# Kernel optimization log

Hardware: AMD Instinct MI355X
Metric: run time of the kernel (lower is better)

The kernel has to match this reference:

```python
import jax, jax.numpy as jnp
import numpy as np

N_BITS = 14
L = 1 << N_BITS
B, C_IN, C_OUT = 32, 32, 64

def _neigh_idx():
    # (L, n_bits): index j flipped at bit b -> j ^ (1<<b)
    s = jnp.arange(L)
    return jnp.stack([s ^ (1 << b) for b in range(N_BITS)], axis=1)

def setup_inputs() -> dict:
    key = jax.random.key(0)
    k1, k2, k3, k4 = jax.random.split(key, 4)
    x = jax.random.normal(k1, (B, C_IN, L), dtype=jnp.float32)
    w_self = jnp.ones((), dtype=jnp.float32)
    w_bits = jax.random.normal(k2, (N_BITS,), dtype=jnp.float32) * 0.1
    # Conv1d(kernel_size=1) weight squeezed to (C_out, C_in)
    mix_w = jax.random.normal(k3, (C_OUT, C_IN), dtype=jnp.float32) * (1.0 / np.sqrt(C_IN))
    mix_b = jax.random.normal(k4, (C_OUT,), dtype=jnp.float32) * 0.01
    return {"x": x, "w_self": w_self, "w_bits": w_bits, "mix_w": mix_w, "mix_b": mix_b}

def reference(x, w_self, w_bits, mix_w, mix_b):
    n_bits = w_bits.shape[0]
    idx = _neigh_idx()                          # (L, n_bits), int32
    xn = x[:, :, idx]                           # (B, C, L, n_bits) XOR-neighbor gather
    neigh_sum = jnp.einsum('bclk,k->bcl', xn, w_bits)
    y = w_self * x + neigh_sum
    y = y / (1.0 + n_bits)                      # agg == 'mean'
    # 1x1 conv mix: (B,C,L) x (C_out,C_in) -> (B,C_out,L)
    return jnp.einsum('bcl,oc->bol', y, mix_w) + mix_b[None, :, None]
```

## Files before the change

### kernel.cpp

```cpp
#include <hip/hip_runtime.h>

#define TILE  256
#define CIN   32
#define COUT  64
#define LSIZE 16384
#define NBITS 14

typedef float f32x4   __attribute__((ext_vector_type(4)));
typedef float vfloat4 __attribute__((ext_vector_type(4)));

__global__ __launch_bounds__(256, 4)
void hamming_fused(const float* __restrict__ x,
                   const float* __restrict__ w_self,
                   const float* __restrict__ w_bits,
                   const float* __restrict__ mix_w,
                   const float* __restrict__ mix_b,
                   float* __restrict__ out)
{
    __shared__ float xs[CIN][TILE];
    __shared__ float mws[CIN][COUT];

    const int tid  = threadIdx.x;
    const int lane = tid & 63;
    const int wv   = tid >> 6;

    const int d    = blockIdx.x;
    const int xcd  = d & 7;
    const int j    = d >> 3;
    const int b    = xcd * 4 + (j >> 6);
    const int tile = j & 63;
    const int base = tile * TILE;
    const float* xb = x + (size_t)b * CIN * LSIZE;

    #pragma unroll
    for (int i = 0; i < (CIN * COUT) / 256; ++i) {
        int g = tid + i * 256;
        int o = g >> 5, c = g & 31;
        mws[c][o] = mix_w[g];
    }

    #pragma unroll
    for (int i = 0; i < 8; ++i) {
        const int r = wv + i * 4;
        const float* src = xb + (size_t)r * LSIZE + base + lane * 4;
        __builtin_amdgcn_global_load_lds(
            (const __attribute__((address_space(1))) void*)src,
            (__attribute__((address_space(3))) void*)&xs[r][lane * 4],
            16, 0, 0);
    }

    const float ws = w_self[0];
    float wb[NBITS];
    #pragma unroll
    for (int k = 0; k < NBITS; ++k) wb[k] = w_bits[k];

    __syncthreads();

    const int c0   = wv * 8;
    const int colb = lane * 4;

    f32x4 yv[8];
    #pragma unroll
    for (int cc = 0; cc < 8; cc += 2) {
        f32x4 pf[2][6];
        #pragma unroll
        for (int u = 0; u < 2; ++u) {
            const float* xr = xb + (size_t)(c0 + cc + u) * LSIZE;
            #pragma unroll
            for (int kk = 0; kk < 6; ++kk)
                pf[u][kk] = *(const f32x4*)(xr + ((base ^ (TILE << kk)) + colb));
        }
        #pragma unroll
        for (int u = 0; u < 2; ++u) {
            const int c = c0 + cc + u;
            const f32x4 s = *(const f32x4*)&xs[c][colb];
            f32x4 a = s * ws;
            a.x += wb[0] * s.y; a.y += wb[0] * s.x; a.z += wb[0] * s.w; a.w += wb[0] * s.z;
            a.x += wb[1] * s.z; a.y += wb[1] * s.w; a.z += wb[1] * s.x; a.w += wb[1] * s.y;
            #pragma unroll
            for (int k = 2; k < 8; ++k) {
                const f32x4 t = *(const f32x4*)&xs[c][colb ^ (1 << k)];
                a += wb[k] * t;
            }
            #pragma unroll
            for (int kk = 0; kk < 6; ++kk)
                a += wb[8 + kk] * pf[u][kk];
            yv[cc + u] = a * (1.0f / 15.0f);
        }
    }
    __syncthreads();

    #pragma unroll
    for (int cc = 0; cc < 8; ++cc)
        *(f32x4*)&xs[c0 + cc][colb] = yv[cc];
    __syncthreads();

    const int tx  = tid & 63;
    const int ty  = tid >> 6;
    const int cb2 = tx << 2;
    const int o0  = ty * 16;

    float4 acc[16];
    #pragma unroll
    for (int jj = 0; jj < 16; ++jj) {
        float bias = mix_b[o0 + jj];
        acc[jj] = make_float4(bias, bias, bias, bias);
    }

    #pragma unroll 4
    for (int c = 0; c < CIN; ++c) {
        float4 yc = *(float4*)&xs[c][cb2];
        #pragma unroll
        for (int j4 = 0; j4 < 4; ++j4) {
            float4 m = *(float4*)&mws[c][o0 + j4 * 4];
            acc[j4*4+0].x += m.x * yc.x; acc[j4*4+0].y += m.x * yc.y;
            acc[j4*4+0].z += m.x * yc.z; acc[j4*4+0].w += m.x * yc.w;
            acc[j4*4+1].x += m.y * yc.x; acc[j4*4+1].y += m.y * yc.y;
            acc[j4*4+1].z += m.y * yc.z; acc[j4*4+1].w += m.y * yc.w;
            acc[j4*4+2].x += m.z * yc.x; acc[j4*4+2].y += m.z * yc.y;
            acc[j4*4+2].z += m.z * yc.z; acc[j4*4+2].w += m.z * yc.w;
            acc[j4*4+3].x += m.w * yc.x; acc[j4*4+3].y += m.w * yc.y;
            acc[j4*4+3].z += m.w * yc.z; acc[j4*4+3].w += m.w * yc.w;
        }
    }

    float* ob = out + (size_t)b * COUT * LSIZE;
    #pragma unroll
    for (int jj = 0; jj < 16; ++jj) {
        vfloat4 v; v.x = acc[jj].x; v.y = acc[jj].y; v.z = acc[jj].z; v.w = acc[jj].w;
        vfloat4* p = (vfloat4*)(ob + (size_t)(o0 + jj) * LSIZE + base + cb2);
        __builtin_nontemporal_store(v, p);
    }
}

extern "C" void kernel_launch(void* const* d_in, const int* in_sizes, int n_in,
                              void* d_out, int out_size, void* d_ws, size_t ws_size,
                              hipStream_t stream) {
    const float* x      = (const float*)d_in[0];
    const float* w_self = (const float*)d_in[1];
    const float* w_bits = (const float*)d_in[2];
    const float* mix_w  = (const float*)d_in[3];
    const float* mix_b  = (const float*)d_in[4];
    float* out = (float*)d_out;

    hamming_fused<<<dim3(2048), 256, 0, stream>>>(x, w_self, w_bits, mix_w, mix_b, out);
}
```

Before: 219.1 us.

## Read mix weights directly from global memory and drop the LDS weight staging

Removes the shared-memory copy of mix_w and its transposed staging loop. The 1x1-conv loop now reads mix_w rows as wave-uniform float4 loads from global memory, likely scalar or cached loads, over four input channels at a time using vector FMAs. The bias is loaded as float4, and launch bounds rise from 4 to 5 blocks per CU since LDS per block shrinks. The cost is weight loads in the inner loop that are no longer unrolled, and extra register pressure under the tighter occupancy target.

```diff
diff --git a/kernel.cpp b/kernel.cpp
--- a/kernel.cpp
+++ b/kernel.cpp
@@ -6,10 +6,14 @@
 #define LSIZE 16384
 #define NBITS 14
 
-typedef float f32x4   __attribute__((ext_vector_type(4)));
-typedef float vfloat4 __attribute__((ext_vector_type(4)));
+typedef float f32x4 __attribute__((ext_vector_type(4)));
 
-__global__ __launch_bounds__(256, 4)
+__device__ __forceinline__ f32x4 splat4(float s) {
+    f32x4 v = {s, s, s, s};
+    return v;
+}
+
+__global__ __launch_bounds__(256, 5)
 void hamming_fused(const float* __restrict__ x,
                    const float* __restrict__ w_self,
                    const float* __restrict__ w_bits,
@@ -18,7 +22,6 @@
                    float* __restrict__ out)
 {
     __shared__ float xs[CIN][TILE];
-    __shared__ float mws[CIN][COUT];
 
     const int tid  = threadIdx.x;
     const int lane = tid & 63;
@@ -31,13 +34,6 @@
     const int tile = j & 63;
     const int base = tile * TILE;
     const float* xb = x + (size_t)b * CIN * LSIZE;
-
-    #pragma unroll
-    for (int i = 0; i < (CIN * COUT) / 256; ++i) {
-        int g = tid + i * 256;
-        int o = g >> 5, c = g & 31;
-        mws[c][o] = mix_w[g];
-    }
 
     #pragma unroll
     for (int i = 0; i < 8; ++i) {
@@ -56,7 +52,7 @@
 
     __syncthreads();
 
-    const int c0   = wv * 8;
+    const int c0ch = wv * 8;
     const int colb = lane * 4;
 
     f32x4 yv[8];
@@ -65,14 +61,14 @@
         f32x4 pf[2][6];
         #pragma unroll
         for (int u = 0; u < 2; ++u) {
-            const float* xr = xb + (size_t)(c0 + cc + u) * LSIZE;
+            const float* xr = xb + (size_t)(c0ch + cc + u) * LSIZE;
             #pragma unroll
             for (int kk = 0; kk < 6; ++kk)
                 pf[u][kk] = *(const f32x4*)(xr + ((base ^ (TILE << kk)) + colb));
         }
         #pragma unroll
         for (int u = 0; u < 2; ++u) {
-            const int c = c0 + cc + u;
+            const int c = c0ch + cc + u;
             const f32x4 s = *(const f32x4*)&xs[c][colb];
             f32x4 a = s * ws;
             a.x += wb[0] * s.y; a.y += wb[0] * s.x; a.z += wb[0] * s.w; a.w += wb[0] * s.z;
@@ -92,7 +88,7 @@
 
     #pragma unroll
     for (int cc = 0; cc < 8; ++cc)
-        *(f32x4*)&xs[c0 + cc][colb] = yv[cc];
+        *(f32x4*)&xs[c0ch + cc][colb] = yv[cc];
     __syncthreads();
 
     const int tx  = tid & 63;
@@ -100,36 +96,38 @@
     const int cb2 = tx << 2;
     const int o0  = ty * 16;
 
-    float4 acc[16];
+    f32x4 acc[16];
     #pragma unroll
-    for (int jj = 0; jj < 16; ++jj) {
-        float bias = mix_b[o0 + jj];
-        acc[jj] = make_float4(bias, bias, bias, bias);
+    for (int q = 0; q < 4; ++q) {
+        const f32x4 b4 = *(const f32x4*)(mix_b + o0 + q * 4);
+        acc[q * 4 + 0] = splat4(b4.x);
+        acc[q * 4 + 1] = splat4(b4.y);
+        acc[q * 4 + 2] = splat4(b4.z);
+        acc[q * 4 + 3] = splat4(b4.w);
     }
 
-    #pragma unroll 4
-    for (int c = 0; c < CIN; ++c) {
-        float4 yc = *(float4*)&xs[c][cb2];
+    #pragma unroll 1
+    for (int c0 = 0; c0 < CIN; c0 += 4) {
+        const f32x4 y0 = *(const f32x4*)&xs[c0 + 0][cb2];
+        const f32x4 y1 = *(const f32x4*)&xs[c0 + 1][cb2];
+        const f32x4 y2 = *(const f32x4*)&xs[c0 + 2][cb2];
+        const f32x4 y3 = *(const f32x4*)&xs[c0 + 3][cb2];
+        const float* wp = mix_w + o0 * CIN + c0;
         #pragma unroll
-        for (int j4 = 0; j4 < 4; ++j4) {
-            float4 m = *(float4*)&mws[c][o0 + j4 * 4];
-            acc[j4*4+0].x += m.x * yc.x; acc[j4*4+0].y += m.x * yc.y;
-            acc[j4*4+0].z += m.x * yc.z; acc[j4*4+0].w += m.x * yc.w;
-            acc[j4*4+1].x += m.y * yc.x; acc[j4*4+1].y += m.y * yc.y;
-            acc[j4*4+1].z += m.y * yc.z; acc[j4*4+1].w += m.y * yc.w;
-            acc[j4*4+2].x += m.z * yc.x; acc[j4*4+2].y += m.z * yc.y;
-            acc[j4*4+2].z += m.z * yc.z; acc[j4*4+2].w += m.z * yc.w;
-            acc[j4*4+3].x += m.w * yc.x; acc[j4*4+3].y += m.w * yc.y;
-            acc[j4*4+3].z += m.w * yc.z; acc[j4*4+3].w += m.w * yc.w;
+        for (int jj = 0; jj < 16; ++jj) {
+            const f32x4 w4 = *(const f32x4*)(wp + jj * CIN);
+            acc[jj] += w4.x * y0;
+            acc[jj] += w4.y * y1;
+            acc[jj] += w4.z * y2;
+            acc[jj] += w4.w * y3;
         }
     }
 
     float* ob = out + (size_t)b * COUT * LSIZE;
     #pragma unroll
     for (int jj = 0; jj < 16; ++jj) {
-        vfloat4 v; v.x = acc[jj].x; v.y = acc[jj].y; v.z = acc[jj].z; v.w = acc[jj].w;
-        vfloat4* p = (vfloat4*)(ob + (size_t)(o0 + jj) * LSIZE + base + cb2);
-        __builtin_nontemporal_store(v, p);
+        f32x4* p = (f32x4*)(ob + (size_t)(o0 + jj) * LSIZE + base + cb2);
+        __builtin_nontemporal_store(acc[jj], p);
     }
 }
 
```

Result: slower. 232.9 us (+6.3%).
